# Kernel tuning notes

Measured on AMD Instinct MI355X. Metric: run time of the kernel, lower is better.

## Reference

```python
import jax, jax.numpy as jnp
import numpy as np

N, E, D = 100000, 400000, 128
LN_EPS = 1e-5
BN_EPS = 1e-5


def layer_norm(v, g, b):
    mu = jnp.mean(v, axis=-1, keepdims=True)
    var = jnp.var(v, axis=-1, keepdims=True)
    return (v - mu) * jax.lax.rsqrt(var + LN_EPS) * g + b


def setup_inputs() -> dict:
    key = jax.random.key(0)
    ks = jax.random.split(key, 12)
    s1 = 1.0 / np.sqrt(2 * D)
    s2 = 1.0 / np.sqrt(D)
    return {
        "x": jax.random.normal(ks[0], (N, D), jnp.float32),
        "edge_attr": jax.random.normal(ks[1], (E, D), jnp.float32),
        "W1": jax.random.uniform(ks[2], (2 * D, D), jnp.float32, -s1, s1),
        "b1": jax.random.uniform(ks[3], (D,), jnp.float32, -s1, s1),
        "g1": jnp.ones((D,), jnp.float32),
        "be1": jnp.zeros((D,), jnp.float32),
        "W2": jax.random.uniform(ks[4], (D, D), jnp.float32, -s2, s2),
        "b2": jax.random.uniform(ks[5], (D,), jnp.float32, -s2, s2),
        "g2": jnp.ones((D,), jnp.float32),
        "be2": jnp.zeros((D,), jnp.float32),
        "W3": jax.random.uniform(ks[6], (D, D), jnp.float32, -s2, s2),
        "b3": jax.random.uniform(ks[7], (D,), jnp.float32, -s2, s2),
        "eps": jnp.zeros((1,), jnp.float32),
        "bn_g": jnp.ones((D,), jnp.float32),
        "bn_b": jnp.zeros((D,), jnp.float32),
        "edge_index": jax.random.randint(ks[8], (2, E), 0, N, jnp.int64),
    }


def reference(x, edge_attr, W1, b1, g1, be1, W2, b2, g2, be2, W3, b3, eps, bn_g, bn_b, edge_index):
    row, col = edge_index[0], edge_index[1]
    identity_outer = x  # in_dim == out_dim -> projections are identity
    # GIN layer
    x_j = x[row]  # [E, D] gather
    xc = jnp.concatenate([x_j, edge_attr], axis=1)  # [E, 2D]
    h = jax.nn.relu(layer_norm(xc @ W1 + b1, g1, be1))  # edge_node_mlp
    agg = jax.ops.segment_sum(h, col, num_segments=x.shape[0])  # scatter_add over col
    out = (1.0 + eps) * x + agg
    out = jax.nn.relu(layer_norm(out @ W2 + b2, g2, be2)) @ W3 + b3  # mlp
    out = out + x  # inner residual (projection is None)
    out = out + identity_outer  # outer residual
    # BatchNorm1d (training mode: batch statistics, biased var)
    mu = jnp.mean(out, axis=0)
    var = jnp.var(out, axis=0)
    out = (out - mu) * jax.lax.rsqrt(var + BN_EPS) * bn_g + bn_b
    return out
```

## Files before the change

### kernel.cpp

```cpp
#include <hip/hip_runtime.h>

#define NN 100000
#define EE 400000

typedef unsigned short u16;
typedef unsigned int u32;
typedef short short8 __attribute__((ext_vector_type(8)));
typedef __bf16 bf16x8 __attribute__((ext_vector_type(8)));
typedef float f32x4 __attribute__((ext_vector_type(4)));

__device__ __forceinline__ short8 pack_bf16x8(f32x4 lo, f32x4 hi) {
  bf16x8 r;
#pragma unroll
  for (int j = 0; j < 4; ++j) { r[j] = (__bf16)lo[j]; r[4 + j] = (__bf16)hi[j]; }
  return __builtin_bit_cast(short8, r);
}

__device__ __forceinline__ u16 f2bf(float f) {
  return __builtin_bit_cast(unsigned short, (__bf16)f);
}

__device__ __forceinline__ float bf2f(short s) {
  u32 b = ((u32)(unsigned short)s) << 16;
  return __builtin_bit_cast(float, b);
}

__global__ void __launch_bounds__(256) k_cast(
    const float* __restrict__ x, u16* __restrict__ xb)
{
  const long total = (long)NN * 16;
  for (long i = (long)blockIdx.x * 256 + threadIdx.x; i < total;
       i += (long)gridDim.x * 256) {
    f32x4 v0 = reinterpret_cast<const f32x4*>(x)[i * 2];
    f32x4 v1 = reinterpret_cast<const f32x4*>(x)[i * 2 + 1];
    reinterpret_cast<short8*>(xb)[i] = pack_bf16x8(v0, v1);
  }
}

__global__ void __launch_bounds__(256) k_hist(
    const int* __restrict__ eidx, int* __restrict__ deg)
{
  for (int e = blockIdx.x * 256 + threadIdx.x; e < EE; e += gridDim.x * 256)
    atomicAdd(&deg[eidx[EE + e]], 1);
}

__global__ void __launch_bounds__(256) k_bsum(
    const int* __restrict__ deg, int* __restrict__ bsum)
{
  const int t = threadIdx.x;
  int idx = blockIdx.x * 1024 + t * 4;
  int s = 0;
#pragma unroll
  for (int i = 0; i < 4; ++i) if (idx + i < NN) s += deg[idx + i];
#pragma unroll
  for (int m = 1; m < 64; m <<= 1) s += __shfl_xor(s, m);
  __shared__ int ws_[4];
  if ((t & 63) == 0) ws_[t >> 6] = s;
  __syncthreads();
  if (t == 0) bsum[blockIdx.x] = ws_[0] + ws_[1] + ws_[2] + ws_[3];
}

__global__ void k_scanb(int* __restrict__ bsum, int* __restrict__ start)
{
  if (threadIdx.x == 0 && blockIdx.x == 0) {
    int run = 0;
    for (int b = 0; b < 98; ++b) { int t = bsum[b]; bsum[b] = run; run += t; }
    start[NN] = EE;
  }
}

__global__ void __launch_bounds__(256) k_scanc(
    const int* __restrict__ deg, const int* __restrict__ bsum,
    int* __restrict__ start, int* __restrict__ cur)
{
  const int t = threadIdx.x, lane = t & 63, wv = t >> 6;
  int idx = blockIdx.x * 1024 + t * 4;
  int c[4], ts = 0;
#pragma unroll
  for (int i = 0; i < 4; ++i) { c[i] = (idx + i < NN) ? deg[idx + i] : 0; ts += c[i]; }
  int incl = ts;
#pragma unroll
  for (int d = 1; d < 64; d <<= 1) {
    int u = __shfl_up(incl, d);
    if (lane >= d) incl += u;
  }
  __shared__ int wsum[4];
  if (lane == 63) wsum[wv] = incl;
  __syncthreads();
  int base = bsum[blockIdx.x];
  for (int w = 0; w < wv; ++w) base += wsum[w];
  int run = base + incl - ts;
#pragma unroll
  for (int i = 0; i < 4; ++i) {
    if (idx + i < NN) { start[idx + i] = run; cur[idx + i] = run; }
    run += c[i];
  }
}

__global__ void __launch_bounds__(256) k_fill(
    const int* __restrict__ eidx, int* __restrict__ cur, int* __restrict__ sid)
{
  for (int e = blockIdx.x * 256 + threadIdx.x; e < EE; e += gridDim.x * 256) {
    int c = eidx[EE + e];
    int p = atomicAdd(&cur[c], 1);
    sid[p] = e;
  }
}

__global__ void __launch_bounds__(512) k_edge(
    const u16* __restrict__ xb, const float* __restrict__ ea,
    const float* __restrict__ W1, const float* __restrict__ b1,
    const float* __restrict__ g1, const float* __restrict__ be1,
    const int* __restrict__ eidx, const int* __restrict__ sid,
    u16* __restrict__ hbuf)
{
  extern __shared__ char smem[];
  const int tid = threadIdx.x;

#pragma unroll
  for (int i = 0; i < 8; ++i) {
    int f = i * 512 + tid;
    int lo_ = f & 15;
    int kb_ = (f >> 4) & 3;
    int kc_ = (f >> 6) & 7;
    int nt_ = f >> 9;
    int n = nt_ * 16 + lo_;
    int k0 = kc_ * 32 + kb_ * 8;
    bf16x8 p;
#pragma unroll
    for (int j = 0; j < 8; ++j) p[j] = (__bf16)W1[(k0 + j) * 128 + n];
    *reinterpret_cast<short8*>(smem + f * 16) = __builtin_bit_cast(short8, p);
  }

  const int lane = tid & 63;
  const int wv = tid >> 6;
  const int lo = lane & 15;
  const int kb = lane >> 4;
  char* tb = smem + 65536 + wv * 4096;

  float b1v[8], g1v[8], bev[8];
#pragma unroll
  for (int nt = 0; nt < 8; ++nt) {
    int c = nt * 16 + lo;
    b1v[nt] = b1[c]; g1v[nt] = g1[c]; bev[nt] = be1[c];
  }
  __syncthreads();

  for (int t = blockIdx.x; t < EE / 128; t += gridDim.x) {
    const int pbase = t * 128 + wv * 16;
    const int p = pbase + lo;
    const int e = sid[p];
    const int r = eidx[e];

    short8 a[8];
#pragma unroll
    for (int kc = 0; kc < 4; ++kc)
      a[kc] = *reinterpret_cast<const short8*>(xb + (long)r * 128 + kc * 32 + kb * 8);
#pragma unroll
    for (int kc = 4; kc < 8; ++kc) {
      const float* src = ea + (long)e * 128 + (kc - 4) * 32 + kb * 8;
      f32x4 v0 = __builtin_nontemporal_load(reinterpret_cast<const f32x4*>(src));
      f32x4 v1 = __builtin_nontemporal_load(reinterpret_cast<const f32x4*>(src) + 1);
      a[kc] = pack_bf16x8(v0, v1);
    }

    f32x4 acc[8];
#pragma unroll
    for (int nt = 0; nt < 8; ++nt) acc[nt] = (f32x4){0.f, 0.f, 0.f, 0.f};

#pragma unroll
    for (int nt = 0; nt < 8; ++nt)
#pragma unroll
      for (int kc = 0; kc < 8; ++kc) {
        short8 b = *reinterpret_cast<const short8*>(
            smem + nt * 8192 + kc * 1024 + lane * 16);
        acc[nt] = __builtin_amdgcn_mfma_f32_16x16x32_bf16(a[kc], b, acc[nt], 0, 0, 0);
      }

    float s[4] = {0.f, 0.f, 0.f, 0.f};
    float q[4] = {0.f, 0.f, 0.f, 0.f};
#pragma unroll
    for (int nt = 0; nt < 8; ++nt)
#pragma unroll
      for (int i = 0; i < 4; ++i) {
        float v = acc[nt][i] + b1v[nt];
        acc[nt][i] = v;
        s[i] += v; q[i] += v * v;
      }
#pragma unroll
    for (int m = 1; m < 16; m <<= 1)
#pragma unroll
      for (int i = 0; i < 4; ++i) {
        s[i] += __shfl_xor(s[i], m);
        q[i] += __shfl_xor(q[i], m);
      }
    float mu[4], rs[4];
#pragma unroll
    for (int i = 0; i < 4; ++i) {
      mu[i] = s[i] * (1.f / 128.f);
      float var = q[i] * (1.f / 128.f) - mu[i] * mu[i];
      rs[i] = rsqrtf(var + 1e-5f);
    }

#pragma unroll
    for (int nt = 0; nt < 8; ++nt)
#pragma unroll
      for (int i = 0; i < 4; ++i) {
        float v = fmaxf((acc[nt][i] - mu[i]) * rs[i] * g1v[nt] + bev[nt], 0.f);
        float vn = __shfl_xor(v, 1);
        if (!(lo & 1)) {
          u32 pk = (u32)f2bf(v) | ((u32)f2bf(vn) << 16);
          *reinterpret_cast<u32*>(tb + (kb * 4 + i) * 256 + (nt * 16 + lo) * 2) = pk;
        }
      }
#pragma unroll
    for (int s4 = 0; s4 < 4; ++s4) {
      short8 rv = *reinterpret_cast<const short8*>(
          tb + (s4 * 4 + (lane >> 4)) * 256 + (lane & 15) * 16);
      __builtin_nontemporal_store(rv,
          reinterpret_cast<short8*>(hbuf + ((long)pbase + s4 * 4 + (lane >> 4)) * 128
                                    + (lane & 15) * 8));
    }
  }
}

__global__ void __launch_bounds__(256) k_node1(
    const float* __restrict__ x, const u16* __restrict__ hbuf,
    const int* __restrict__ start,
    const float* __restrict__ W2, const float* __restrict__ b2,
    const float* __restrict__ g2, const float* __restrict__ be2,
    const float* __restrict__ epsp, u16* __restrict__ t1)
{
  __shared__ char smem[32768];
  const int tid = threadIdx.x;
#pragma unroll
  for (int i = 0; i < 8; ++i) {
    int f = i * 256 + tid;
    int lo_ = f & 15;
    int kb_ = (f >> 4) & 3;
    int kc_ = (f >> 6) & 3;
    int nt_ = f >> 8;
    int n = nt_ * 16 + lo_;
    int k0 = kc_ * 32 + kb_ * 8;
    bf16x8 p;
#pragma unroll
    for (int j = 0; j < 8; ++j) p[j] = (__bf16)W2[(k0 + j) * 128 + n];
    *reinterpret_cast<short8*>(smem + f * 16) = __builtin_bit_cast(short8, p);
  }

  const int lane = tid & 63, wv = tid >> 6, lo = lane & 15, kb = lane >> 4;
  const float ope = 1.f + epsp[0];
  __syncthreads();

  const int row = blockIdx.x * 64 + wv * 16 + lo;
  const int rc = row < NN ? row : NN - 1;

  float uacc[4][8];
#pragma unroll
  for (int kc = 0; kc < 4; ++kc)
#pragma unroll
    for (int j = 0; j < 8; ++j) uacc[kc][j] = 0.f;

  const int p0 = start[rc], p1 = start[rc + 1];
  for (int p = p0; p < p1; ++p) {
    const u16* hr = hbuf + (long)p * 128 + kb * 8;
#pragma unroll
    for (int kc = 0; kc < 4; ++kc) {
      short8 hv = __builtin_nontemporal_load(
          reinterpret_cast<const short8*>(hr + kc * 32));
#pragma unroll
      for (int j = 0; j < 8; ++j) uacc[kc][j] += bf2f(hv[j]);
    }
  }

  short8 a[4];
#pragma unroll
  for (int kc = 0; kc < 4; ++kc) {
    const float* xp = x + (long)rc * 128 + kc * 32 + kb * 8;
    f32x4 x0 = *reinterpret_cast<const f32x4*>(xp);
    f32x4 x1 = *reinterpret_cast<const f32x4*>(xp + 4);
    f32x4 u0, u1;
#pragma unroll
    for (int j = 0; j < 4; ++j) {
      u0[j] = fmaf(x0[j], ope, uacc[kc][j]);
      u1[j] = fmaf(x1[j], ope, uacc[kc][4 + j]);
    }
    a[kc] = pack_bf16x8(u0, u1);
  }

  f32x4 acc[8];
#pragma unroll
  for (int nt = 0; nt < 8; ++nt) acc[nt] = (f32x4){0.f, 0.f, 0.f, 0.f};

#pragma unroll
  for (int nt = 0; nt < 8; ++nt)
#pragma unroll
    for (int kc = 0; kc < 4; ++kc) {
      short8 b = *reinterpret_cast<const short8*>(smem + nt * 4096 + kc * 1024 + lane * 16);
      acc[nt] = __builtin_amdgcn_mfma_f32_16x16x32_bf16(a[kc], b, acc[nt], 0, 0, 0);
    }

  float b2v[8], g2v[8], bev[8];
#pragma unroll
  for (int nt = 0; nt < 8; ++nt) {
    int c = nt * 16 + lo;
    b2v[nt] = b2[c]; g2v[nt] = g2[c]; bev[nt] = be2[c];
  }

  float s[4] = {0.f, 0.f, 0.f, 0.f};
  float q[4] = {0.f, 0.f, 0.f, 0.f};
#pragma unroll
  for (int nt = 0; nt < 8; ++nt)
#pragma unroll
    for (int i = 0; i < 4; ++i) {
      float v = acc[nt][i] + b2v[nt];
      acc[nt][i] = v;
      s[i] += v; q[i] += v * v;
    }
#pragma unroll
  for (int m = 1; m < 16; m <<= 1)
#pragma unroll
    for (int i = 0; i < 4; ++i) {
      s[i] += __shfl_xor(s[i], m);
      q[i] += __shfl_xor(q[i], m);
    }
  float mu[4], rs[4];
  int rows[4];
#pragma unroll
  for (int i = 0; i < 4; ++i) {
    mu[i] = s[i] * (1.f / 128.f);
    float var = q[i] * (1.f / 128.f) - mu[i] * mu[i];
    rs[i] = rsqrtf(var + 1e-5f);
    rows[i] = blockIdx.x * 64 + wv * 16 + kb * 4 + i;
  }
#pragma unroll
  for (int nt = 0; nt < 8; ++nt)
#pragma unroll
    for (int i = 0; i < 4; ++i) {
      float v = fmaxf((acc[nt][i] - mu[i]) * rs[i] * g2v[nt] + bev[nt], 0.f);
      float vn = __shfl_xor(v, 1);
      if (!(lo & 1) && rows[i] < NN) {
        u32 pk = (u32)f2bf(v) | ((u32)f2bf(vn) << 16);
        *reinterpret_cast<u32*>(t1 + (long)rows[i] * 128 + nt * 16 + lo) = pk;
      }
    }
}

__global__ void __launch_bounds__(256) k_node2(
    const u16* __restrict__ t1, const float* __restrict__ x,
    const float* __restrict__ W3, const float* __restrict__ b3,
    float* __restrict__ tmp, float* __restrict__ part)
{
  __shared__ char smem[32768];
  const int tid = threadIdx.x;
#pragma unroll
  for (int i = 0; i < 8; ++i) {
    int f = i * 256 + tid;
    int lo_ = f & 15;
    int kb_ = (f >> 4) & 3;
    int kc_ = (f >> 6) & 3;
    int nt_ = f >> 8;
    int n = nt_ * 16 + lo_;
    int k0 = kc_ * 32 + kb_ * 8;
    bf16x8 p;
#pragma unroll
    for (int j = 0; j < 8; ++j) p[j] = (__bf16)W3[(k0 + j) * 128 + n];
    *reinterpret_cast<short8*>(smem + f * 16) = __builtin_bit_cast(short8, p);
  }
  __syncthreads();

  const int lane = tid & 63, wv = tid >> 6, lo = lane & 15, kb = lane >> 4;
  const long rb = (long)blockIdx.x * 128 + wv * 32;

  short8 a[2][4];
#pragma unroll
  for (int mt = 0; mt < 2; ++mt) {
    long row = rb + mt * 16 + lo;
    long rc = row < NN ? row : (NN - 1);
#pragma unroll
    for (int kc = 0; kc < 4; ++kc)
      a[mt][kc] = *reinterpret_cast<const short8*>(t1 + rc * 128 + kc * 32 + kb * 8);
  }

  f32x4 acc[2][8];
#pragma unroll
  for (int mt = 0; mt < 2; ++mt)
#pragma unroll
    for (int nt = 0; nt < 8; ++nt)
      acc[mt][nt] = (f32x4){0.f, 0.f, 0.f, 0.f};

#pragma unroll
  for (int nt = 0; nt < 8; ++nt)
#pragma unroll
    for (int kc = 0; kc < 4; ++kc) {
      short8 b = *reinterpret_cast<const short8*>(smem + nt * 4096 + kc * 1024 + lane * 16);
      acc[0][nt] = __builtin_amdgcn_mfma_f32_16x16x32_bf16(a[0][kc], b, acc[0][nt], 0, 0, 0);
      acc[1][nt] = __builtin_amdgcn_mfma_f32_16x16x32_bf16(a[1][kc], b, acc[1][nt], 0, 0, 0);
    }

  float b3v[8];
#pragma unroll
  for (int nt = 0; nt < 8; ++nt) b3v[nt] = b3[nt * 16 + lo];

  float sn[8] = {0.f, 0.f, 0.f, 0.f, 0.f, 0.f, 0.f, 0.f};
  float qn[8] = {0.f, 0.f, 0.f, 0.f, 0.f, 0.f, 0.f, 0.f};

#pragma unroll
  for (int mt = 0; mt < 2; ++mt) {
    long rows[4], rc[4];
    bool val[4];
#pragma unroll
    for (int i = 0; i < 4; ++i) {
      rows[i] = rb + mt * 16 + kb * 4 + i;
      val[i] = rows[i] < NN;
      rc[i] = val[i] ? rows[i] : (NN - 1);
    }
#pragma unroll
    for (int nt = 0; nt < 8; ++nt)
#pragma unroll
      for (int i = 0; i < 4; ++i) {
        float v = acc[mt][nt][i] + b3v[nt] + 2.f * x[rc[i] * 128 + nt * 16 + lo];
        if (val[i]) {
          tmp[rows[i] * 128 + nt * 16 + lo] = v;
          sn[nt] += v; qn[nt] += v * v;
        }
      }
  }
#pragma unroll
  for (int nt = 0; nt < 8; ++nt) {
    sn[nt] += __shfl_xor(sn[nt], 16); sn[nt] += __shfl_xor(sn[nt], 32);
    qn[nt] += __shfl_xor(qn[nt], 16); qn[nt] += __shfl_xor(qn[nt], 32);
  }
  if (lane < 16) {
    long pr = ((long)blockIdx.x * 4 + wv) * 256;
#pragma unroll
    for (int nt = 0; nt < 8; ++nt) {
      part[pr + nt * 16 + lane] = sn[nt];
      part[pr + 128 + nt * 16 + lane] = qn[nt];
    }
  }
}

__global__ void __launch_bounds__(256) k_stats(
    const float* __restrict__ part, const float* __restrict__ bng,
    const float* __restrict__ bnb, float* __restrict__ stats2)
{
  const int c = blockIdx.x;
  const int tid = threadIdx.x;
  float s = 0.f, q = 0.f;
  for (int i = tid; i < 3128; i += 256) {
    s += part[(long)i * 256 + c];
    q += part[(long)i * 256 + 128 + c];
  }
#pragma unroll
  for (int m = 1; m < 64; m <<= 1) { s += __shfl_xor(s, m); q += __shfl_xor(q, m); }
  __shared__ float rs_[4], rq_[4];
  const int wv = tid >> 6;
  if ((tid & 63) == 0) { rs_[wv] = s; rq_[wv] = q; }
  __syncthreads();
  if (tid == 0) {
    s = rs_[0] + rs_[1] + rs_[2] + rs_[3];
    q = rq_[0] + rq_[1] + rq_[2] + rq_[3];
    float mu = s * (1.f / (float)NN);
    float var = q * (1.f / (float)NN) - mu * mu;
    float sc = rsqrtf(var + 1e-5f) * bng[c];
    stats2[c] = sc;
    stats2[128 + c] = bnb[c] - mu * sc;
  }
}

__global__ void __launch_bounds__(256) k_apply(
    const float* __restrict__ tmp, const float* __restrict__ stats2,
    float* __restrict__ out)
{
  const long total = (long)NN * 32;
  for (long i = (long)blockIdx.x * 256 + threadIdx.x; i < total;
       i += (long)gridDim.x * 256) {
    int db = (int)((i & 31) << 2);
    f32x4 v = reinterpret_cast<const f32x4*>(tmp)[i];
    f32x4 sc = *reinterpret_cast<const f32x4*>(stats2 + db);
    f32x4 sh = *reinterpret_cast<const f32x4*>(stats2 + 128 + db);
    f32x4 o;
#pragma unroll
    for (int j = 0; j < 4; ++j) o[j] = fmaf(v[j], sc[j], sh[j]);
    reinterpret_cast<f32x4*>(out)[i] = o;
  }
}

extern "C" void kernel_launch(void* const* d_in, const int* in_sizes, int n_in,
                              void* d_out, int out_size, void* d_ws, size_t ws_size,
                              hipStream_t stream)
{
  const float* x   = (const float*)d_in[0];
  const float* ea  = (const float*)d_in[1];
  const float* W1  = (const float*)d_in[2];
  const float* b1  = (const float*)d_in[3];
  const float* g1  = (const float*)d_in[4];
  const float* be1 = (const float*)d_in[5];
  const float* W2  = (const float*)d_in[6];
  const float* b2  = (const float*)d_in[7];
  const float* g2  = (const float*)d_in[8];
  const float* be2 = (const float*)d_in[9];
  const float* W3  = (const float*)d_in[10];
  const float* b3  = (const float*)d_in[11];
  const float* eps = (const float*)d_in[12];
  const float* bng = (const float*)d_in[13];
  const float* bnb = (const float*)d_in[14];
  const int*   eidx = (const int*)d_in[15];
  float* out = (float*)d_out;

  u16*   hbuf   = (u16*)d_ws;
  u16*   t1     = (u16*)((char*)d_ws + 102400000L);
  u16*   xb     = t1;
  float* tmp    = (float*)d_ws;
  float* part   = (float*)((char*)d_ws + 128000000L);
  float* stats2 = part + 3128L * 256;
  int*   deg    = (int*)(stats2 + 256);
  int*   start  = deg + NN;
  int*   cur    = start + NN + 1;
  int*   bsum   = cur + NN;
  int*   sid    = bsum + 128;

  (void)hipFuncSetAttribute(reinterpret_cast<const void*>(k_edge),
                            hipFuncAttributeMaxDynamicSharedMemorySize, 98304);

  hipMemsetAsync(deg, 0, (size_t)NN * 4, stream);
  k_cast  <<<1024, 256, 0, stream>>>(x, xb);
  k_hist  <<<512, 256, 0, stream>>>(eidx, deg);
  k_bsum  <<<98, 256, 0, stream>>>(deg, bsum);
  k_scanb <<<1, 64, 0, stream>>>(bsum, start);
  k_scanc <<<98, 256, 0, stream>>>(deg, bsum, start, cur);
  k_fill  <<<512, 256, 0, stream>>>(eidx, cur, sid);
  k_edge  <<<256, 512, 98304, stream>>>(xb, ea, W1, b1, g1, be1, eidx, sid, hbuf);
  k_node1 <<<(NN + 63) / 64, 256, 0, stream>>>(x, hbuf, start, W2, b2, g2, be2, eps, t1);
  k_node2 <<<(NN + 127) / 128, 256, 0, stream>>>(t1, x, W3, b3, tmp, part);
  k_stats <<<128, 256, 0, stream>>>(part, bng, bnb, stats2);
  k_apply <<<2048, 256, 0, stream>>>(tmp, stats2, out);
}
```

Measured before the change: 275.7 us.

## Halve edge staging smem, double edge grid, store pre-BN tmp as bf16

The edge kernel's per-wave LDS staging tile is halved: results are written and flushed in two halves, so dynamic shared memory drops and the grid doubles to 512 blocks for more resident blocks. Separately, the pre-BatchNorm intermediate is stored as packed bf16 instead of fp32, which halves the write traffic in node2 and the read traffic in the apply kernel. The bf16 intermediate loses precision before normalization, while the statistics are still taken from the fp32 values.

```diff
diff --git a/kernel.cpp b/kernel.cpp
--- a/kernel.cpp
+++ b/kernel.cpp
@@ -136,7 +136,7 @@
   const int wv = tid >> 6;
   const int lo = lane & 15;
   const int kb = lane >> 4;
-  char* tb = smem + 65536 + wv * 4096;
+  char* tb = smem + 65536 + wv * 2048;
 
   float b1v[8], g1v[8], bev[8];
 #pragma unroll
@@ -202,24 +202,35 @@
       rs[i] = rsqrtf(var + 1e-5f);
     }
 
+    u32 pk[8][4];
 #pragma unroll
     for (int nt = 0; nt < 8; ++nt)
 #pragma unroll
       for (int i = 0; i < 4; ++i) {
         float v = fmaxf((acc[nt][i] - mu[i]) * rs[i] * g1v[nt] + bev[nt], 0.f);
         float vn = __shfl_xor(v, 1);
-        if (!(lo & 1)) {
-          u32 pk = (u32)f2bf(v) | ((u32)f2bf(vn) << 16);
-          *reinterpret_cast<u32*>(tb + (kb * 4 + i) * 256 + (nt * 16 + lo) * 2) = pk;
-        }
-      }
-#pragma unroll
-    for (int s4 = 0; s4 < 4; ++s4) {
-      short8 rv = *reinterpret_cast<const short8*>(
-          tb + (s4 * 4 + (lane >> 4)) * 256 + (lane & 15) * 16);
-      __builtin_nontemporal_store(rv,
-          reinterpret_cast<short8*>(hbuf + ((long)pbase + s4 * 4 + (lane >> 4)) * 128
-                                    + (lane & 15) * 8));
+        pk[nt][i] = (u32)f2bf(v) | ((u32)f2bf(vn) << 16);
+      }
+
+#pragma unroll
+    for (int h = 0; h < 2; ++h) {
+      if (h) asm volatile("s_waitcnt lgkmcnt(0)" ::: "memory");
+      if ((kb >> 1) == h && !(lo & 1)) {
+        int rl = (kb & 1) * 4;
+#pragma unroll
+        for (int nt = 0; nt < 8; ++nt)
+#pragma unroll
+          for (int i = 0; i < 4; ++i)
+            *reinterpret_cast<u32*>(tb + (rl + i) * 256 + (nt * 16 + lo) * 2) = pk[nt][i];
+      }
+#pragma unroll
+      for (int s4 = 0; s4 < 2; ++s4) {
+        short8 rv = *reinterpret_cast<const short8*>(
+            tb + (s4 * 4 + (lane >> 4)) * 256 + (lane & 15) * 16);
+        __builtin_nontemporal_store(rv,
+            reinterpret_cast<short8*>(hbuf + ((long)pbase + h * 8 + s4 * 4 + (lane >> 4)) * 128
+                                      + (lane & 15) * 8));
+      }
     }
   }
 }
@@ -349,7 +360,7 @@
 __global__ void __launch_bounds__(256) k_node2(
     const u16* __restrict__ t1, const float* __restrict__ x,
     const float* __restrict__ W3, const float* __restrict__ b3,
-    float* __restrict__ tmp, float* __restrict__ part)
+    u16* __restrict__ tmp, float* __restrict__ part)
 {
   __shared__ char smem[32768];
   const int tid = threadIdx.x;
@@ -420,9 +431,11 @@
 #pragma unroll
       for (int i = 0; i < 4; ++i) {
         float v = acc[mt][nt][i] + b3v[nt] + 2.f * x[rc[i] * 128 + nt * 16 + lo];
-        if (val[i]) {
-          tmp[rows[i] * 128 + nt * 16 + lo] = v;
-          sn[nt] += v; qn[nt] += v * v;
+        if (val[i]) { sn[nt] += v; qn[nt] += v * v; }
+        float vn = __shfl_xor(v, 1);
+        if (!(lo & 1) && val[i]) {
+          u32 pk = (u32)f2bf(v) | ((u32)f2bf(vn) << 16);
+          *reinterpret_cast<u32*>(tmp + rows[i] * 128 + nt * 16 + lo) = pk;
         }
       }
   }
@@ -470,20 +483,26 @@
 }
 
 __global__ void __launch_bounds__(256) k_apply(
-    const float* __restrict__ tmp, const float* __restrict__ stats2,
+    const u16* __restrict__ tmp, const float* __restrict__ stats2,
     float* __restrict__ out)
 {
-  const long total = (long)NN * 32;
+  const long total = (long)NN * 16;
   for (long i = (long)blockIdx.x * 256 + threadIdx.x; i < total;
        i += (long)gridDim.x * 256) {
-    int db = (int)((i & 31) << 2);
-    f32x4 v = reinterpret_cast<const f32x4*>(tmp)[i];
-    f32x4 sc = *reinterpret_cast<const f32x4*>(stats2 + db);
-    f32x4 sh = *reinterpret_cast<const f32x4*>(stats2 + 128 + db);
-    f32x4 o;
-#pragma unroll
-    for (int j = 0; j < 4; ++j) o[j] = fmaf(v[j], sc[j], sh[j]);
-    reinterpret_cast<f32x4*>(out)[i] = o;
+    int db = (int)((i & 15) << 3);
+    short8 hv = reinterpret_cast<const short8*>(tmp)[i];
+    f32x4 sc0 = *reinterpret_cast<const f32x4*>(stats2 + db);
+    f32x4 sc1 = *reinterpret_cast<const f32x4*>(stats2 + db + 4);
+    f32x4 sh0 = *reinterpret_cast<const f32x4*>(stats2 + 128 + db);
+    f32x4 sh1 = *reinterpret_cast<const f32x4*>(stats2 + 128 + db + 4);
+    f32x4 o0, o1;
+#pragma unroll
+    for (int j = 0; j < 4; ++j) {
+      o0[j] = fmaf(bf2f(hv[j]), sc0[j], sh0[j]);
+      o1[j] = fmaf(bf2f(hv[4 + j]), sc1[j], sh1[j]);
+    }
+    reinterpret_cast<f32x4*>(out)[i * 2] = o0;
+    reinterpret_cast<f32x4*>(out)[i * 2 + 1] = o1;
   }
 }
 
@@ -512,7 +531,7 @@
   u16*   hbuf   = (u16*)d_ws;
   u16*   t1     = (u16*)((char*)d_ws + 102400000L);
   u16*   xb     = t1;
-  float* tmp    = (float*)d_ws;
+  u16*   tmp    = (u16*)d_ws;
   float* part   = (float*)((char*)d_ws + 128000000L);
   float* stats2 = part + 3128L * 256;
   int*   deg    = (int*)(stats2 + 256);
@@ -522,7 +541,7 @@
   int*   sid    = bsum + 128;
 
   (void)hipFuncSetAttribute(reinterpret_cast<const void*>(k_edge),
-                            hipFuncAttributeMaxDynamicSharedMemorySize, 98304);
+                            hipFuncAttributeMaxDynamicSharedMemorySize, 81920);
 
   hipMemsetAsync(deg, 0, (size_t)NN * 4, stream);
   k_cast  <<<1024, 256, 0, stream>>>(x, xb);
@@ -531,7 +550,7 @@
   k_scanb <<<1, 64, 0, stream>>>(bsum, start);
   k_scanc <<<98, 256, 0, stream>>>(deg, bsum, start, cur);
   k_fill  <<<512, 256, 0, stream>>>(eidx, cur, sid);
-  k_edge  <<<256, 512, 98304, stream>>>(xb, ea, W1, b1, g1, be1, eidx, sid, hbuf);
+  k_edge  <<<512, 512, 81920, stream>>>(xb, ea, W1, b1, g1, be1, eidx, sid, hbuf);
   k_node1 <<<(NN + 63) / 64, 256, 0, stream>>>(x, hbuf, start, W2, b2, g2, be2, eps, t1);
   k_node2 <<<(NN + 127) / 128, 256, 0, stream>>>(t1, x, W3, b3, tmp, part);
   k_stats <<<128, 256, 0, stream>>>(part, bng, bnb, stats2);
```

After: 269.6 us. 1.02x faster.
